# Kernel optimization log

Hardware: AMD Instinct MI355X
Metric: run time of the kernel (lower is better)

Reference implementation:

```python
import jax, jax.numpy as jnp
import numpy as np

N_EXPERTS = 16
D_IN = 2048
D_OUT = 2048
BATCH = 4096


def setup_inputs() -> dict:
    key = jax.random.key(0)
    k_x, k_m, k_a, k_w, k_b = jax.random.split(key, 5)
    xs = jax.random.normal(k_x, (BATCH, D_IN), dtype=jnp.float32)
    mxs = jax.random.normal(k_m, (BATCH,), dtype=jnp.float32)
    actions = jax.random.randint(k_a, (BATCH,), 0, N_EXPERTS, dtype=jnp.int64)
    # Per-expert Linear params: W[e] is [d_out, d_in], b[e] is [d_out]
    scale = 1.0 / np.sqrt(D_IN)
    W = jax.random.uniform(k_w, (N_EXPERTS, D_OUT, D_IN), dtype=jnp.float32,
                           minval=-scale, maxval=scale)
    b = jax.random.uniform(k_b, (N_EXPERTS, D_OUT), dtype=jnp.float32,
                           minval=-scale, maxval=scale)
    return {"xs": xs, "mxs": mxs, "actions": actions, "W": W, "b": b}


def reference(xs, mxs, actions, W, b):
    # Original: per-sample dispatch y[i] = submodule[actions[i]](x[i]).
    # Grouped form: for each expert e, run the full-batch GEMM and combine
    # with a mask (fixed small loop over experts; no data-dim Python loop).
    ys = jnp.zeros((xs.shape[0], W.shape[1]), dtype=xs.dtype)
    for e in range(W.shape[0]):
        ye = xs @ W[e].T + b[e]                      # [B, d_out]
        mask = (actions == e)[:, None]               # [B, 1]
        ys = jnp.where(mask, ye, ys)
    return (ys, mxs, actions)
```

## Files before the change

kernel.cpp:

```cpp
#include <hip/hip_runtime.h>
#include <hip/hip_bf16.h>

#define BATCH 4096
#define NEXP  16
#define DIN   2048
#define DOUT  2048

#define BM 128
#define BN 64
#define NKT 64

#define WS_X_OFF   65536
#define PADROWS    4352
#define WS_X_BYTES ((size_t)PADROWS * 4096)

typedef __attribute__((ext_vector_type(4))) float f32x4;
typedef __attribute__((ext_vector_type(8))) short bf16x8;

__global__ void sort_kernel(const int* __restrict__ actions,
                            const float* __restrict__ mxs,
                            float* __restrict__ out_tail,
                            int* __restrict__ offs,
                            int* __restrict__ poffs,
                            int* __restrict__ sorted) {
    __shared__ int s_cnt[NEXP];
    __shared__ int s_cur[NEXP];
    const int tid = threadIdx.x;
    if (tid < NEXP) s_cnt[tid] = 0;
    __syncthreads();
    for (int i = tid; i < BATCH; i += blockDim.x) {
        int a = actions[i];
        atomicAdd(&s_cnt[a], 1);
        out_tail[i] = mxs[i];
        out_tail[BATCH + i] = (float)a;
    }
    __syncthreads();
    if (tid == 0) {
        int run = 0, prun = 0;
        for (int e = 0; e < NEXP; ++e) {
            offs[e] = run;  s_cur[e] = run;
            poffs[e] = prun;
            run += s_cnt[e];
            prun += (s_cnt[e] + 15) & ~15;
        }
        offs[NEXP] = run;
        poffs[NEXP] = prun;
    }
    __syncthreads();
    for (int i = tid; i < BATCH; i += blockDim.x) {
        int e = actions[i];
        int pos = atomicAdd(&s_cur[e], 1);
        sorted[pos] = i;
    }
}

__device__ __forceinline__ unsigned rne2(float x0, float x1) {
    unsigned b0 = __float_as_uint(x0), b1 = __float_as_uint(x1);
    b0 = b0 + 0x7FFFu + ((b0 >> 16) & 1u);
    b1 = b1 + 0x7FFFu + ((b1 >> 16) & 1u);
    return (b1 & 0xFFFF0000u) | (b0 >> 16);
}

__device__ __forceinline__ int lidx32(int r, int kb) {
    return r * 32 + ((kb ^ ((r >> 1) & 3)) << 3);
}

__device__ __forceinline__ int lidx(int r, int kb) {
    return r * 64 + ((kb ^ (r & 7)) << 3);
}

__global__ void xsplit_kernel(const float* __restrict__ xs,
                              const int* __restrict__ sorted,
                              const int* __restrict__ offs,
                              const int* __restrict__ poffs,
                              unsigned char* __restrict__ xws) {
    const int t = threadIdx.x;
    const int slot = t & 15;
    const int ktq = t >> 4;
    const int p = blockIdx.x * 16 + slot;
    if (p >= poffs[NEXP]) return;
    int e = 0;
#pragma unroll
    for (int i = 1; i < NEXP; ++i)
        if (p >= poffs[i]) e = i;
    const int local = p - poffs[e];
    if (local >= offs[e + 1] - offs[e]) return;
    const int src = sorted[offs[e] + local];
    const float* srow = xs + (size_t)src * DIN;
    unsigned char* gbase = xws + (size_t)blockIdx.x * 65536;
#pragma unroll
    for (int q = 0; q < 4; ++q) {
        const int kt = ktq * 4 + q;
        const float* s = srow + kt * 32;
        uint4 L[4];
#pragma unroll
        for (int j = 0; j < 4; ++j) {
            float4 a = *(const float4*)(s + 8 * j);
            float4 b = *(const float4*)(s + 8 * j + 4);
            L[j].x = rne2(a.x, a.y); L[j].y = rne2(a.z, a.w);
            L[j].z = rne2(b.x, b.y); L[j].w = rne2(b.z, b.w);
        }
        unsigned char* d = gbase + kt * 1024 + slot * 16;
#pragma unroll
        for (int g = 0; g < 4; ++g)
            *(uint4*)(d + g * 256) = L[g];
    }
}

__global__ __launch_bounds__(256, 4)
void gemm_kernel(const unsigned char* __restrict__ xws,
                 const float* __restrict__ W,
                 const float* __restrict__ bias,
                 const int* __restrict__ offs,
                 const int* __restrict__ poffs,
                 const int* __restrict__ sorted,
                 float* __restrict__ out) {
    __shared__ __align__(16) unsigned short Wl[2][BN * 32];

    const int e = blockIdx.y;
    const int start = offs[e];
    const int cnt = offs[e + 1] - start;
    const int m0 = blockIdx.z * BM;
    if (m0 >= cnt) return;
    const int n0 = blockIdx.x * BN;

    const int tid = threadIdx.x;
    const int lane = tid & 63;
    const int wave = tid >> 6;
    const int g = lane >> 4, rl = lane & 15;

    const int swr = tid >> 2;
    const int wkq = tid & 3;
    const float* wsrc = W + ((size_t)e * DOUT + n0 + swr) * DIN + wkq * 8;

    const unsigned char* xb[2];
#pragma unroll
    for (int mi = 0; mi < 2; ++mi) {
        int prow = poffs[e] + m0 + wave * 32 + mi * 16;
        if (prow > PADROWS - 16) prow = PADROWS - 16;
        xb[mi] = xws + ((size_t)prow >> 4) * 65536 + (size_t)lane * 16;
    }

    f32x4 acc[2][4];
#pragma unroll
    for (int i = 0; i < 2; ++i)
#pragma unroll
        for (int j = 0; j < 4; ++j) acc[i][j] = (f32x4){0.f, 0.f, 0.f, 0.f};

    float4 pwA[2], pwB[2];
    pwA[0] = *(const float4*)(wsrc);
    pwA[1] = *(const float4*)(wsrc + 4);
    pwB[0] = *(const float4*)(wsrc + 32);
    pwB[1] = *(const float4*)(wsrc + 32 + 4);
    bf16x8 axA[2], axB[2];
#pragma unroll
    for (int mi = 0; mi < 2; ++mi)
        axA[mi] = *(const bf16x8*)(xb[mi]);
    {
        uint4 u;
        u.x = rne2(pwA[0].x, pwA[0].y); u.y = rne2(pwA[0].z, pwA[0].w);
        u.z = rne2(pwA[1].x, pwA[1].y); u.w = rne2(pwA[1].z, pwA[1].w);
        *(uint4*)&Wl[0][lidx32(swr, wkq)] = u;
        pwA[0] = *(const float4*)(wsrc + 2 * 32);
        pwA[1] = *(const float4*)(wsrc + 2 * 32 + 4);
    }

    int kt = 0;

#define KSTEP(AXC, AXN, PWU, PAR) do {                                         \
    __builtin_amdgcn_sched_barrier(0);                                         \
    asm volatile("s_waitcnt lgkmcnt(0)" ::: "memory");                         \
    __builtin_amdgcn_sched_barrier(0);                                         \
    __builtin_amdgcn_s_barrier();                                              \
    __builtin_amdgcn_sched_barrier(0);                                         \
    bf16x8 bh[4];                                                              \
    _Pragma("unroll")                                                          \
    for (int ni = 0; ni < 4; ++ni)                                             \
        bh[ni] = *(const bf16x8*)&Wl[PAR][lidx32(ni * 16 + rl, g)];            \
    {      \
      int _kn = (kt + 1) & (NKT - 1);                                          \
      _Pragma("unroll")                                                        \
      for (int mi = 0; mi < 2; ++mi)                                           \
          AXN[mi] = *(const bf16x8*)(xb[mi] + _kn * 1024); }                   \
    {                             \
      uint4 u;                                                                 \
      u.x = rne2(PWU[0].x, PWU[0].y); u.y = rne2(PWU[0].z, PWU[0].w);          \
      u.z = rne2(PWU[1].x, PWU[1].y); u.w = rne2(PWU[1].z, PWU[1].w);          \
      *(uint4*)&Wl[PAR ^ 1][lidx32(swr, wkq)] = u; }                           \
    {                                             \
      int _k3 = (kt + 3) & (NKT - 1);                                          \
      PWU[0] = *(const float4*)(wsrc + _k3 * 32);                              \
      PWU[1] = *(const float4*)(wsrc + _k3 * 32 + 4); }                        \
    __builtin_amdgcn_s_setprio(1);                                             \
    _Pragma("unroll")                                                          \
    for (int mi = 0; mi < 2; ++mi)                                             \
        _Pragma("unroll")                                                      \
        for (int ni = 0; ni < 4; ++ni)                                         \
            acc[mi][ni] = __builtin_amdgcn_mfma_f32_16x16x32_bf16(AXC[mi], bh[ni], acc[mi][ni], 0, 0, 0); \
    __builtin_amdgcn_s_setprio(0);                                             \
    ++kt;                                                                      \
} while (0)

#pragma unroll 1
    for (int it = 0; it < NKT / 2; ++it) {
        KSTEP(axA, axB, pwB, 0);
        KSTEP(axB, axA, pwA, 1);
    }
#undef KSTEP

    float bv[4];
#pragma unroll
    for (int ni = 0; ni < 4; ++ni)
        bv[ni] = bias[(size_t)e * DOUT + n0 + ni * 16 + rl];
#pragma unroll
    for (int mi = 0; mi < 2; ++mi) {
#pragma unroll
        for (int j = 0; j < 4; ++j) {
            int rm = m0 + wave * 32 + mi * 16 + g * 4 + j;
            if (rm < cnt) {
                int s = sorted[start + rm];
                float* orow = out + (size_t)s * DOUT + n0 + rl;
#pragma unroll
                for (int ni = 0; ni < 4; ++ni)
                    orow[ni * 16] = acc[mi][ni][j] + bv[ni];
            }
        }
    }
}

__device__ __forceinline__ void split_pair(float x0, float x1, unsigned& h, unsigned& l) {
    unsigned b0 = __float_as_uint(x0), b1 = __float_as_uint(x1);
    unsigned h0 = b0 & 0xFFFF0000u;
    unsigned h1 = b1 & 0xFFFF0000u;
    h = h1 | (b0 >> 16);
    unsigned l0 = __float_as_uint(x0 - __uint_as_float(h0));
    unsigned l1 = __float_as_uint(x1 - __uint_as_float(h1));
    l = (l1 & 0xFFFF0000u) | (l0 >> 16);
}
__device__ __forceinline__ void split_f4pair(float4 a, float4 b, uint4& h, uint4& l) {
    split_pair(a.x, a.y, h.x, l.x);
    split_pair(a.z, a.w, h.y, l.y);
    split_pair(b.x, b.y, h.z, l.z);
    split_pair(b.z, b.w, h.w, l.w);
}

__global__ __launch_bounds__(256, 3)
void gemm_fb(const float* __restrict__ xs,
             const float* __restrict__ W,
             const float* __restrict__ bias,
             const int* __restrict__ offs,
             const int* __restrict__ sorted,
             float* __restrict__ out) {
    __shared__ __align__(16) unsigned short Xs[128 * 64];
    __shared__ __align__(16) unsigned short Ws[64 * 64];

    const int e = blockIdx.y;
    const int start = offs[e];
    const int cnt = offs[e + 1] - start;
    const int m0 = blockIdx.z * 128;
    if (m0 >= cnt) return;
    const int n0 = blockIdx.x * 64;

    const int tid = threadIdx.x;
    const int lane = tid & 63;
    const int wave = tid >> 6;
    const int wm = wave >> 1, wn = wave & 1;
    const int srow = tid & 127, kq = tid >> 7;
    const int swr = tid >> 2, wkq = tid & 3;

    const int rm_s = m0 + srow;
    const int xrow = (rm_s < cnt) ? sorted[start + rm_s] : -1;
    const float* xsrc = xs + (size_t)(xrow < 0 ? 0 : xrow) * DIN + kq * 16;
    const float* wsrc = W + ((size_t)e * DOUT + n0 + swr) * DIN + wkq * 8;

    f32x4 acc[4][2];
#pragma unroll
    for (int i = 0; i < 4; ++i)
#pragma unroll
        for (int j = 0; j < 2; ++j) acc[i][j] = (f32x4){0.f, 0.f, 0.f, 0.f};

    float4 px[4], pw[2];
#pragma unroll
    for (int j = 0; j < 4; ++j)
        px[j] = (xrow >= 0) ? *(const float4*)(xsrc + j * 4) : make_float4(0.f, 0.f, 0.f, 0.f);
    pw[0] = *(const float4*)(wsrc);
    pw[1] = *(const float4*)(wsrc + 4);

    for (int k0 = 0; k0 < DIN; k0 += 32) {
        {
            uint4 xh0, xl0, xh1, xl1, wh, wl;
            split_f4pair(px[0], px[1], xh0, xl0);
            split_f4pair(px[2], px[3], xh1, xl1);
            split_f4pair(pw[0], pw[1], wh, wl);
            *(uint4*)&Xs[lidx(srow, 2 * kq)]         = xh0;
            *(uint4*)&Xs[lidx(srow, 2 * kq + 1)]     = xh1;
            *(uint4*)&Xs[lidx(srow, 4 + 2 * kq)]     = xl0;
            *(uint4*)&Xs[lidx(srow, 4 + 2 * kq + 1)] = xl1;
            *(uint4*)&Ws[lidx(swr, wkq)]             = wh;
            *(uint4*)&Ws[lidx(swr, 4 + wkq)]         = wl;
        }
        __syncthreads();
        {
            int kn = (k0 + 32 < DIN) ? (k0 + 32) : 0;
#pragma unroll
            for (int j = 0; j < 4; ++j)
                px[j] = (xrow >= 0) ? *(const float4*)(xsrc + kn + j * 4) : make_float4(0.f, 0.f, 0.f, 0.f);
            pw[0] = *(const float4*)(wsrc + kn);
            pw[1] = *(const float4*)(wsrc + kn + 4);
        }
        {
            const int gg = lane >> 4, rrl = lane & 15;
            bf16x8 ah[4], al[4], bh[2], bl[2];
#pragma unroll
            for (int mi = 0; mi < 4; ++mi) {
                int R = wm * 64 + mi * 16 + rrl;
                ah[mi] = *(const bf16x8*)&Xs[lidx(R, gg)];
                al[mi] = *(const bf16x8*)&Xs[lidx(R, 4 + gg)];
            }
#pragma unroll
            for (int ni = 0; ni < 2; ++ni) {
                int R = wn * 32 + ni * 16 + rrl;
                bh[ni] = *(const bf16x8*)&Ws[lidx(R, gg)];
                bl[ni] = *(const bf16x8*)&Ws[lidx(R, 4 + gg)];
            }
#pragma unroll
            for (int mi = 0; mi < 4; ++mi)
#pragma unroll
                for (int ni = 0; ni < 2; ++ni)
                    acc[mi][ni] = __builtin_amdgcn_mfma_f32_16x16x32_bf16(ah[mi], bh[ni], acc[mi][ni], 0, 0, 0);
#pragma unroll
            for (int mi = 0; mi < 4; ++mi)
#pragma unroll
                for (int ni = 0; ni < 2; ++ni)
                    acc[mi][ni] = __builtin_amdgcn_mfma_f32_16x16x32_bf16(ah[mi], bl[ni], acc[mi][ni], 0, 0, 0);
#pragma unroll
            for (int mi = 0; mi < 4; ++mi)
#pragma unroll
                for (int ni = 0; ni < 2; ++ni)
                    acc[mi][ni] = __builtin_amdgcn_mfma_f32_16x16x32_bf16(al[mi], bh[ni], acc[mi][ni], 0, 0, 0);
        }
        __syncthreads();
    }

    const int gg = lane >> 4, rrl = lane & 15;
    float bv[2];
#pragma unroll
    for (int ni = 0; ni < 2; ++ni)
        bv[ni] = bias[(size_t)e * DOUT + n0 + wn * 32 + ni * 16 + rrl];
#pragma unroll
    for (int mi = 0; mi < 4; ++mi) {
#pragma unroll
        for (int j = 0; j < 4; ++j) {
            int rm = m0 + wm * 64 + mi * 16 + gg * 4 + j;
            if (rm < cnt) {
                int s = sorted[start + rm];
                float* orow = out + (size_t)s * DOUT + n0 + wn * 32 + rrl;
#pragma unroll
                for (int ni = 0; ni < 2; ++ni)
                    orow[ni * 16] = acc[mi][ni][j] + bv[ni];
            }
        }
    }
}

extern "C" void kernel_launch(void* const* d_in, const int* in_sizes, int n_in,
                              void* d_out, int out_size, void* d_ws, size_t ws_size,
                              hipStream_t stream) {
    const float* xs      = (const float*)d_in[0];
    const float* mxs     = (const float*)d_in[1];
    const int*   actions = (const int*)d_in[2];
    const float* W       = (const float*)d_in[3];
    const float* b       = (const float*)d_in[4];
    float* out = (float*)d_out;

    int* ws_i   = (int*)d_ws;
    int* offs   = ws_i;
    int* poffs  = ws_i + 20;
    int* sorted = ws_i + 64;

    sort_kernel<<<1, 1024, 0, stream>>>(actions, mxs,
                                        out + (size_t)BATCH * DOUT,
                                        offs, poffs, sorted);

    if (ws_size >= WS_X_OFF + WS_X_BYTES) {
        unsigned char* xws = (unsigned char*)d_ws + WS_X_OFF;
        xsplit_kernel<<<PADROWS / 16, 256, 0, stream>>>(xs, sorted, offs, poffs, xws);
        dim3 grid(DOUT / BN, NEXP, BATCH / BM);
        gemm_kernel<<<grid, 256, 0, stream>>>(xws, W, b, offs, poffs, sorted, out);
    } else {
        dim3 grid(DOUT / 64, NEXP, BATCH / 128);
        gemm_fb<<<grid, 256, 0, stream>>>(xs, W, b, offs, sorted, out);
    }
}
```

Before: 163.6 us.

## Double K-step depth per barrier in expert GEMM main loop

Each pipeline stage of the GEMM loop now covers 64 K elements instead of 32. The W LDS tile doubles to 64 columns with a new XOR swizzle, each thread loads twice as many W and X fragments, and 16 MFMAs run per barrier instead of 8. This halves the number of LDS barriers and waitcnt stalls over the K loop. In exchange, register and LDS use rise and the launch bound drops from 4 to 3 blocks per CU, so occupancy may fall.

```diff
diff --git a/kernel.cpp b/kernel.cpp
--- a/kernel.cpp
+++ b/kernel.cpp
@@ -9,6 +9,7 @@
 #define BM 128
 #define BN 64
 #define NKT 64
+#define NPAIR 32
 
 #define WS_X_OFF   65536
 #define PADROWS    4352
@@ -61,8 +62,8 @@
     return (b1 & 0xFFFF0000u) | (b0 >> 16);
 }
 
-__device__ __forceinline__ int lidx32(int r, int kb) {
-    return r * 32 + ((kb ^ ((r >> 1) & 3)) << 3);
+__device__ __forceinline__ int lidxW(int r, int kb) {
+    return r * 64 + ((kb ^ (r & 7)) << 3);
 }
 
 __device__ __forceinline__ int lidx(int r, int kb) {
@@ -107,7 +108,7 @@
     }
 }
 
-__global__ __launch_bounds__(256, 4)
+__global__ __launch_bounds__(256, 3)
 void gemm_kernel(const unsigned char* __restrict__ xws,
                  const float* __restrict__ W,
                  const float* __restrict__ bias,
@@ -115,7 +116,7 @@
                  const int* __restrict__ poffs,
                  const int* __restrict__ sorted,
                  float* __restrict__ out) {
-    __shared__ __align__(16) unsigned short Wl[2][BN * 32];
+    __shared__ __align__(16) unsigned short Wl[2][BN * 64];
 
     const int e = blockIdx.y;
     const int start = offs[e];
@@ -131,7 +132,7 @@
 
     const int swr = tid >> 2;
     const int wkq = tid & 3;
-    const float* wsrc = W + ((size_t)e * DOUT + n0 + swr) * DIN + wkq * 8;
+    const float* wsrc = W + ((size_t)e * DOUT + n0 + swr) * DIN + wkq * 16;
 
     const unsigned char* xb[2];
 #pragma unroll
@@ -147,62 +148,77 @@
 #pragma unroll
         for (int j = 0; j < 4; ++j) acc[i][j] = (f32x4){0.f, 0.f, 0.f, 0.f};
 
-    float4 pwA[2], pwB[2];
-    pwA[0] = *(const float4*)(wsrc);
-    pwA[1] = *(const float4*)(wsrc + 4);
-    pwB[0] = *(const float4*)(wsrc + 32);
-    pwB[1] = *(const float4*)(wsrc + 32 + 4);
-    bf16x8 axA[2], axB[2];
-#pragma unroll
-    for (int mi = 0; mi < 2; ++mi)
-        axA[mi] = *(const bf16x8*)(xb[mi]);
+    float4 pwA[4], pwB[4];
+#pragma unroll
+    for (int j = 0; j < 4; ++j) pwA[j] = *(const float4*)(wsrc + 0 * 64 + 4 * j);
+#pragma unroll
+    for (int j = 0; j < 4; ++j) pwB[j] = *(const float4*)(wsrc + 1 * 64 + 4 * j);
+    bf16x8 axA[2][2], axB[2][2];
+#pragma unroll
+    for (int mi = 0; mi < 2; ++mi) {
+        axA[mi][0] = *(const bf16x8*)(xb[mi]);
+        axA[mi][1] = *(const bf16x8*)(xb[mi] + 1024);
+    }
     {
-        uint4 u;
-        u.x = rne2(pwA[0].x, pwA[0].y); u.y = rne2(pwA[0].z, pwA[0].w);
-        u.z = rne2(pwA[1].x, pwA[1].y); u.w = rne2(pwA[1].z, pwA[1].w);
-        *(uint4*)&Wl[0][lidx32(swr, wkq)] = u;
-        pwA[0] = *(const float4*)(wsrc + 2 * 32);
-        pwA[1] = *(const float4*)(wsrc + 2 * 32 + 4);
-    }
-
-    int kt = 0;
+        uint4 u0, u1;
+        u0.x = rne2(pwA[0].x, pwA[0].y); u0.y = rne2(pwA[0].z, pwA[0].w);
+        u0.z = rne2(pwA[1].x, pwA[1].y); u0.w = rne2(pwA[1].z, pwA[1].w);
+        u1.x = rne2(pwA[2].x, pwA[2].y); u1.y = rne2(pwA[2].z, pwA[2].w);
+        u1.z = rne2(pwA[3].x, pwA[3].y); u1.w = rne2(pwA[3].z, pwA[3].w);
+        *(uint4*)&Wl[0][lidxW(swr, 2 * wkq)]     = u0;
+        *(uint4*)&Wl[0][lidxW(swr, 2 * wkq + 1)] = u1;
+#pragma unroll
+        for (int j = 0; j < 4; ++j) pwA[j] = *(const float4*)(wsrc + 2 * 64 + 4 * j);
+    }
+
+    int pr = 0;
 
 #define KSTEP(AXC, AXN, PWU, PAR) do {                                         \
     __builtin_amdgcn_sched_barrier(0);                                         \
-    asm volatile("s_waitcnt lgkmcnt(0)" ::: "memory");                         \
+    asm volatile("s_waitcnt lgkmcnt(0)");                                      \
     __builtin_amdgcn_sched_barrier(0);                                         \
     __builtin_amdgcn_s_barrier();                                              \
     __builtin_amdgcn_sched_barrier(0);                                         \
-    bf16x8 bh[4];                                                              \
+    bf16x8 bh[2][4];                                                           \
     _Pragma("unroll")                                                          \
-    for (int ni = 0; ni < 4; ++ni)                                             \
-        bh[ni] = *(const bf16x8*)&Wl[PAR][lidx32(ni * 16 + rl, g)];            \
-    {      \
-      int _kn = (kt + 1) & (NKT - 1);                                          \
+    for (int j = 0; j < 2; ++j)                                                \
+        _Pragma("unroll")                                                      \
+        for (int ni = 0; ni < 4; ++ni)                                         \
+            bh[j][ni] = *(const bf16x8*)&Wl[PAR][lidxW(ni * 16 + rl, j * 4 + g)]; \
+    {                   \
+      int _kn = ((pr + 1) & (NPAIR - 1)) * 2;                                  \
       _Pragma("unroll")                                                        \
-      for (int mi = 0; mi < 2; ++mi)                                           \
-          AXN[mi] = *(const bf16x8*)(xb[mi] + _kn * 1024); }                   \
-    {                             \
-      uint4 u;                                                                 \
-      u.x = rne2(PWU[0].x, PWU[0].y); u.y = rne2(PWU[0].z, PWU[0].w);          \
-      u.z = rne2(PWU[1].x, PWU[1].y); u.w = rne2(PWU[1].z, PWU[1].w);          \
-      *(uint4*)&Wl[PAR ^ 1][lidx32(swr, wkq)] = u; }                           \
-    {                                             \
-      int _k3 = (kt + 3) & (NKT - 1);                                          \
-      PWU[0] = *(const float4*)(wsrc + _k3 * 32);                              \
-      PWU[1] = *(const float4*)(wsrc + _k3 * 32 + 4); }                        \
+      for (int mi = 0; mi < 2; ++mi) {                                         \
+          AXN[mi][0] = *(const bf16x8*)(xb[mi] + (size_t)_kn * 1024);          \
+          AXN[mi][1] = *(const bf16x8*)(xb[mi] + (size_t)(_kn + 1) * 1024);    \
+      } }                                                                      \
+    {                      \
+      uint4 u0, u1;                                                            \
+      u0.x = rne2(PWU[0].x, PWU[0].y); u0.y = rne2(PWU[0].z, PWU[0].w);        \
+      u0.z = rne2(PWU[1].x, PWU[1].y); u0.w = rne2(PWU[1].z, PWU[1].w);        \
+      u1.x = rne2(PWU[2].x, PWU[2].y); u1.y = rne2(PWU[2].z, PWU[2].w);        \
+      u1.z = rne2(PWU[3].x, PWU[3].y); u1.w = rne2(PWU[3].z, PWU[3].w);        \
+      *(uint4*)&Wl[PAR ^ 1][lidxW(swr, 2 * wkq)]     = u0;                     \
+      *(uint4*)&Wl[PAR ^ 1][lidxW(swr, 2 * wkq + 1)] = u1; }                   \
+    {                                        \
+      int _k3 = (pr + 3) & (NPAIR - 1);                                        \
+      _Pragma("unroll")                                                        \
+      for (int j = 0; j < 4; ++j)                                              \
+          PWU[j] = *(const float4*)(wsrc + (size_t)_k3 * 64 + 4 * j); }        \
     __builtin_amdgcn_s_setprio(1);                                             \
     _Pragma("unroll")                                                          \
-    for (int mi = 0; mi < 2; ++mi)                                             \
+    for (int j = 0; j < 2; ++j)                                                \
         _Pragma("unroll")                                                      \
-        for (int ni = 0; ni < 4; ++ni)                                         \
-            acc[mi][ni] = __builtin_amdgcn_mfma_f32_16x16x32_bf16(AXC[mi], bh[ni], acc[mi][ni], 0, 0, 0); \
+        for (int mi = 0; mi < 2; ++mi)                                         \
+            _Pragma("unroll")                                                  \
+            for (int ni = 0; ni < 4; ++ni)                                     \
+                acc[mi][ni] = __builtin_amdgcn_mfma_f32_16x16x32_bf16(AXC[mi][j], bh[j][ni], acc[mi][ni], 0, 0, 0); \
     __builtin_amdgcn_s_setprio(0);                                             \
-    ++kt;                                                                      \
+    ++pr;                                                                      \
 } while (0)
 
 #pragma unroll 1
-    for (int it = 0; it < NKT / 2; ++it) {
+    for (int it = 0; it < NPAIR / 2; ++it) {
         KSTEP(axA, axB, pwB, 0);
         KSTEP(axB, axA, pwA, 1);
     }
```

Result: no change. 163.9 us (+0.1%).
